# Kernel tuning notes

Hardware: AMD Instinct MI355X
Metric: run time of the kernel (lower is better)

The kernel has to match this reference:

```python
import jax, jax.numpy as jnp
import numpy as np

B, S, D, MP, NA, NC = 32, 1024, 256, 9, 8, 53  # batch, seq, d_model, max_players, n_actions, card vocab


def setup_inputs() -> dict:
    key = jax.random.key(0)
    ks = jax.random.split(key, 24)
    inp = {
        "cards": jax.random.randint(ks[0], (B, S, 7), 0, NC),          # 5 table + 2 hand ids (52 = pad)
        "hero_pos": jax.random.randint(ks[1], (B, S), 0, MP),
        "acting_pos": jax.random.randint(ks[2], (B, S), 0, MP),
        "num_players": jax.random.randint(ks[3], (B, S), 0, MP + 1),
        "scalars": jax.random.normal(ks[4], (B, S, 2), jnp.float32),   # [pot, stack]
        "blinds": jax.random.normal(ks[5], (B, S, 2), jnp.float32),    # [big, small]
        "bets": jax.random.normal(ks[6], (B, S, MP), jnp.float32),
        "action": jax.random.normal(ks[7], (B, S, NA), jnp.float32),
        "mask": jnp.ones((B, S), jnp.float32),
    }
    w = 0.02
    inp.update({
        "card_table": jax.random.normal(ks[8], (NC, D), jnp.float32) * w,
        "hero_table": jax.random.normal(ks[9], (MP, D), jnp.float32) * w,
        "acting_table": jax.random.normal(ks[10], (MP, D), jnp.float32) * w,
        "nump_table": jax.random.normal(ks[11], (MP + 1, D), jnp.float32) * w,
        "scalar_W": jax.random.normal(ks[12], (D, 2), jnp.float32) * w,
        "scalar_b": jax.random.normal(ks[13], (D,), jnp.float32) * w,
        "blind_W": jax.random.normal(ks[14], (D, 2), jnp.float32) * w,
        "blind_b": jax.random.normal(ks[15], (D,), jnp.float32) * w,
        "bet_W": jax.random.normal(ks[16], (D, MP), jnp.float32) * w,
        "bet_b": jax.random.normal(ks[17], (D,), jnp.float32) * w,
        "action_W": jax.random.normal(ks[18], (D, NA), jnp.float32) * w,
        "action_b": jax.random.normal(ks[19], (D,), jnp.float32) * w,
        "combine_W": jax.random.normal(ks[20], (D, 8 * D), jnp.float32) * w,
        "combine_b": jax.random.normal(ks[21], (D,), jnp.float32) * w,
    })
    return inp


def reference(cards, hero_pos, acting_pos, num_players, scalars, blinds, bets, action, mask,
              card_table, hero_table, acting_table, nump_table,
              scalar_W, scalar_b, blind_W, blind_b, bet_W, bet_b,
              action_W, action_b, combine_W, combine_b):
    # Batched gathers (replacing per-event nn.Embedding calls)
    card_emb = card_table[cards].mean(axis=2)          # [B,S,D]
    hero_emb = hero_table[hero_pos]                    # [B,S,D]
    acting_emb = acting_table[acting_pos]              # [B,S,D]
    nump_emb = nump_table[num_players]                 # [B,S,D]
    # Small linear projections (nn.Linear: x @ W.T + b)
    scalar_emb = jnp.einsum('bsk,dk->bsd', scalars, scalar_W) + scalar_b
    blind_emb = jnp.einsum('bsk,dk->bsd', blinds, blind_W) + blind_b
    bet_emb = jnp.einsum('bsk,dk->bsd', bets, bet_W) + bet_b
    action_emb = jnp.einsum('bsk,dk->bsd', action, action_W) + action_b
    # Concat order matches torch: card, hero, acting, scalar, bet, action, num_players, blind
    combined = jnp.concatenate(
        [card_emb, hero_emb, acting_emb, scalar_emb, bet_emb, action_emb, nump_emb, blind_emb],
        axis=-1)                                       # [B,S,8D]
    out = jnp.einsum('bsk,dk->bsd', combined, combine_W) + combine_b  # [B,S,D]
    return out * mask[..., None]                       # zero padded positions
```

## Files before the change

kernel.cpp:

```cpp
#include <hip/hip_runtime.h>

#define D 256
#define W8 2048

#define BPART_OFF 0
#define TBT_OFF   1024
#define KS 136

typedef float nf4  __attribute__((ext_vector_type(4)));
typedef float f32x4 __attribute__((ext_vector_type(4)));
typedef short short8 __attribute__((ext_vector_type(8)));
typedef short short8a2 __attribute__((ext_vector_type(8), aligned(2)));

__device__ __forceinline__ ushort bf16rne(float v) {
    const unsigned x = __float_as_uint(v);
    return (ushort)((x + 0x7fffu + ((x >> 16) & 1u)) >> 16);
}


__global__ __launch_bounds__(256) void fuse5_kernel(
    const float* __restrict__ combine_W,
    const float* __restrict__ card_t, const float* __restrict__ hero_t,
    const float* __restrict__ act_t,  const float* __restrict__ nump_t,
    const float* __restrict__ scalar_W, const float* __restrict__ scalar_b,
    const float* __restrict__ blind_W,  const float* __restrict__ blind_b,
    const float* __restrict__ bet_W,    const float* __restrict__ bet_b,
    const float* __restrict__ action_W, const float* __restrict__ action_b,
    float* __restrict__ ws)
{
    __shared__ float vsh[D];
    __shared__ float Wl[D * 33];

    const int job = blockIdx.x;
    const int tid = threadIdx.x;

    int wblk;
    float scale = 1.0f;
    int kind, orow;

    if (job < 81) {
        kind = 0; orow = job;
        const float* src;
        if (job < 53)      { src = card_t + job * D;        wblk = 0; scale = 1.0f / 7.0f; }
        else if (job < 62) { src = hero_t + (job - 53) * D; wblk = 1; }
        else if (job < 71) { src = act_t  + (job - 62) * D; wblk = 2; }
        else               { src = nump_t + (job - 71) * D; wblk = 6; }
        vsh[tid] = src[tid];
    } else if (job < 102) {
        kind = 1; orow = job - 81;
        const float* secW; int nk, k;
        if (orow < 2)       { secW = scalar_W; nk = 2; k = orow;      wblk = 3; }
        else if (orow < 11) { secW = bet_W;    nk = 9; k = orow - 2;  wblk = 4; }
        else if (orow < 19) { secW = action_W; nk = 8; k = orow - 11; wblk = 5; }
        else                { secW = blind_W;  nk = 2; k = orow - 19; wblk = 7; }
        vsh[tid] = secW[tid * nk + k];
    } else {
        kind = 2; orow = job - 102;
        const float* secB;
        switch (orow) {
            case 0:  secB = scalar_b; wblk = 3; break;
            case 1:  secB = bet_b;    wblk = 4; break;
            case 2:  secB = action_b; wblk = 5; break;
            default: secB = blind_b;  wblk = 7; break;
        }
        vsh[tid] = secB[tid];
    }

    const float* Wbase = combine_W + wblk * D;
    float acc = 0.f;

    for (int t = 0; t < 8; ++t) {
        const int k0 = t * 32;
        __syncthreads();
#pragma unroll
        for (int i = 0; i < 8; ++i) {
            const int fidx = tid + i * 256;
            const int dd = fidx >> 3;
            const int kq = (fidx & 7) * 4;
            const float4 w = *(const float4*)(Wbase + (size_t)dd * W8 + k0 + kq);
            float* p = Wl + dd * 33 + kq;
            p[0] = w.x; p[1] = w.y; p[2] = w.z; p[3] = w.w;
        }
        __syncthreads();
        const float* wrow = Wl + tid * 33;
#pragma unroll
        for (int kk = 0; kk < 32; kk += 4) {
            const float4 vv = *(const float4*)(vsh + k0 + kk);
            acc += wrow[kk]     * vv.x + wrow[kk + 1] * vv.y
                 + wrow[kk + 2] * vv.z + wrow[kk + 3] * vv.w;
        }
    }

    ushort* tbT = (ushort*)(ws + TBT_OFF);
    float*  bpl = ws + BPART_OFF;
    if (kind == 0)      tbT[(size_t)tid * KS + orow]      = bf16rne(acc * scale);
    else if (kind == 1) tbT[(size_t)tid * KS + 81 + orow] = bf16rne(acc);
    else                bpl[orow * D + tid] = acc;
}


#define GEMM_THREADS 256

struct Feat {
    int   c[7], ho, ao, no;
    float fs0, fs1, fb[9], fa[8], fl0, fl1, m;
};

__device__ __forceinline__ void preload(
    int q, int tok, int ok,
    const int* __restrict__ cards,  const int* __restrict__ hero,
    const int* __restrict__ acting, const int* __restrict__ nump,
    const float* __restrict__ scalars, const float* __restrict__ blinds,
    const float* __restrict__ bets,    const float* __restrict__ action,
    const float* __restrict__ mask, Feat& f)
{
    if (!ok) { f.m = 0.f; return; }
    if (q == 0) {
        const int* cp = cards + (size_t)tok * 7;
#pragma unroll
        for (int j = 0; j < 7; ++j) f.c[j] = cp[j];
        f.ho = hero[tok]; f.ao = acting[tok]; f.no = nump[tok];
        f.m = mask[tok];
    } else if (q == 1) {
        const float2 s = *(const float2*)(scalars + (size_t)tok * 2);
        f.fs0 = s.x; f.fs1 = s.y;
        const float* fb = bets + (size_t)tok * 9;
#pragma unroll
        for (int k = 0; k < 9; ++k) f.fb[k] = fb[k];
    } else if (q == 2) {
        const float* fa = action + (size_t)tok * 8;
#pragma unroll
        for (int k = 0; k < 8; ++k) f.fa[k] = fa[k];
        const float2 l = *(const float2*)(blinds + (size_t)tok * 2);
        f.fl0 = l.x; f.fl1 = l.y;
    }
}

__device__ __forceinline__ void writeF(int q, int t, int ok, const Feat& f,
                                       ushort* __restrict__ Fl, float* __restrict__ msk)
{
    ushort* Fr = Fl + t * KS;
    if (q == 0) {
        if (ok) {
            int cnt[7];
#pragma unroll
            for (int j = 0; j < 7; ++j) {
                int n = 1;
#pragma unroll
                for (int i = 0; i < 7; ++i)
                    if (i != j) n += (f.c[i] == f.c[j]) ? 1 : 0;
                cnt[j] = n;
            }
#pragma unroll
            for (int j = 0; j < 7; ++j)
                Fr[f.c[j]] = bf16rne((float)cnt[j]);
            Fr[53 + f.ho] = 0x3F80;
            Fr[62 + f.ao] = 0x3F80;
            Fr[71 + f.no] = 0x3F80;
        }
        msk[t] = f.m;
    } else if (q == 1 && ok) {
        Fr[81] = bf16rne(f.fs0); Fr[82] = bf16rne(f.fs1);
#pragma unroll
        for (int k = 0; k < 9; ++k) Fr[83 + k] = bf16rne(f.fb[k]);
    } else if (q == 2 && ok) {
#pragma unroll
        for (int k = 0; k < 8; ++k) Fr[92 + k] = bf16rne(f.fa[k]);
        Fr[100] = bf16rne(f.fl0); Fr[101] = bf16rne(f.fl1);
    }
}

__device__ __forceinline__ void mfma_tile(
    const ushort* __restrict__ Tg,
    const ushort* __restrict__ Fl,
    const float* __restrict__ msk, const float* __restrict__ bsh,
    int tok0, int h, int w, int lr, int lg,
    float* __restrict__ out, int ntok)
{
    const int nbase = (w >> 1) * 2;
    const int mbase = (w & 1) * 4;

    f32x4 acc[2][4];
#pragma unroll
    for (int nt = 0; nt < 2; ++nt)
#pragma unroll
        for (int mt = 0; mt < 4; ++mt) acc[nt][mt] = (f32x4){0.f, 0.f, 0.f, 0.f};

#pragma unroll
    for (int kt = 0; kt < 4; ++kt) {
        const short8 b0 = *(const short8*)(Fl + ((nbase + 0) * 16 + lr) * KS + kt * 32 + lg * 8);
        const short8 b1 = *(const short8*)(Fl + ((nbase + 1) * 16 + lr) * KS + kt * 32 + lg * 8);
#pragma unroll
        for (int mt = 0; mt < 4; ++mt) {
            const short8 a = *(const short8a2*)(Tg + (size_t)((mbase + mt) * 16 + lr) * KS + kt * 32 + lg * 8);
            acc[0][mt] = __builtin_amdgcn_mfma_f32_16x16x32_bf16(a, b0, acc[0][mt], 0, 0, 0);
            acc[1][mt] = __builtin_amdgcn_mfma_f32_16x16x32_bf16(a, b1, acc[1][mt], 0, 0, 0);
        }
    }

#pragma unroll
    for (int nt = 0; nt < 2; ++nt) {
        const int trow = (nbase + nt) * 16 + lr;
        const int tok = tok0 + trow;
        if (tok < ntok) {
            const float m = msk[trow];
#pragma unroll
            for (int mt = 0; mt < 4; ++mt) {
                const int c = (mbase + mt) * 16 + lg * 4;
                const float4 bb = *(const float4*)(bsh + c);
                nf4 o;
                o.x = (acc[nt][mt][0] + bb.x) * m;
                o.y = (acc[nt][mt][1] + bb.y) * m;
                o.z = (acc[nt][mt][2] + bb.z) * m;
                o.w = (acc[nt][mt][3] + bb.w) * m;
                __builtin_nontemporal_store(o, (nf4*)(out + (size_t)tok * D + h * 128 + c));
            }
        }
    }
}

__global__ __launch_bounds__(GEMM_THREADS) void gemm_kernel(
    const int* __restrict__ cards,  const int* __restrict__ hero,
    const int* __restrict__ acting, const int* __restrict__ nump,
    const float* __restrict__ scalars, const float* __restrict__ blinds,
    const float* __restrict__ bets,    const float* __restrict__ action,
    const float* __restrict__ mask,    const float* __restrict__ combine_b,
    const float* __restrict__ ws, float* __restrict__ out, int ntok)
{
    __shared__ __align__(16) ushort Fl[64 * KS];
    __shared__ float msk[64];
    __shared__ float bsh[128];

    const int tid  = threadIdx.x;
    const int h    = blockIdx.x & 1;
    const int tile = blockIdx.x >> 1;
    const int tok0 = tile * 64;

    const int q = tid >> 6;
    const int t = tid & 63;

    const ushort* Tg = (const ushort*)(ws + TBT_OFF) + (size_t)h * 128 * KS;

    {
        uint* fz = (uint*)Fl;
        for (int i = tid; i < 64 * KS / 2; i += GEMM_THREADS) fz[i] = 0;
        if (tid < 128) {
            const int c = h * 128 + tid;
            bsh[tid] = combine_b[c]
                + ws[BPART_OFF + 0 * D + c] + ws[BPART_OFF + 1 * D + c]
                + ws[BPART_OFF + 2 * D + c] + ws[BPART_OFF + 3 * D + c];
        }
    }
    Feat f;
    preload(q, tok0 + t, tok0 + t < ntok, cards, hero, acting, nump,
            scalars, blinds, bets, action, mask, f);
    __syncthreads();

    writeF(q, t, tok0 + t < ntok, f, Fl, msk);
    __syncthreads();

    const int w  = tid >> 6;
    const int l  = tid & 63;
    const int lr = l & 15;
    const int lg = l >> 4;
    mfma_tile(Tg, Fl, msk, bsh, tok0, h, w, lr, lg, out, ntok);
}

extern "C" void kernel_launch(void* const* d_in, const int* in_sizes, int n_in,
                              void* d_out, int out_size, void* d_ws, size_t ws_size,
                              hipStream_t stream) {
    const int*   cards    = (const int*)d_in[0];
    const int*   hero     = (const int*)d_in[1];
    const int*   acting   = (const int*)d_in[2];
    const int*   nump     = (const int*)d_in[3];
    const float* scalars  = (const float*)d_in[4];
    const float* blinds   = (const float*)d_in[5];
    const float* bets     = (const float*)d_in[6];
    const float* action   = (const float*)d_in[7];
    const float* mask     = (const float*)d_in[8];
    const float* card_t   = (const float*)d_in[9];
    const float* hero_t   = (const float*)d_in[10];
    const float* act_t    = (const float*)d_in[11];
    const float* nump_t   = (const float*)d_in[12];
    const float* scalar_W = (const float*)d_in[13];
    const float* scalar_b = (const float*)d_in[14];
    const float* blind_W  = (const float*)d_in[15];
    const float* blind_b  = (const float*)d_in[16];
    const float* bet_W    = (const float*)d_in[17];
    const float* bet_b    = (const float*)d_in[18];
    const float* action_W = (const float*)d_in[19];
    const float* action_b = (const float*)d_in[20];
    const float* combine_W= (const float*)d_in[21];
    const float* combine_b= (const float*)d_in[22];

    float* ws  = (float*)d_ws;
    float* out = (float*)d_out;
    const int ntok = in_sizes[1];

    const int ntiles = (ntok + 63) / 64;

    hipLaunchKernelGGL(fuse5_kernel, dim3(106), dim3(256), 0, stream,
                       combine_W, card_t, hero_t, act_t, nump_t,
                       scalar_W, scalar_b, blind_W, blind_b, bet_W, bet_b,
                       action_W, action_b, ws);
    hipLaunchKernelGGL(gemm_kernel, dim3(ntiles * 2), dim3(GEMM_THREADS), 0, stream,
                       cards, hero, acting, nump, scalars, blinds, bets, action, mask,
                       combine_b, ws, out, ntok);
}
```

Before: 25.94 us.

## Compute full output width per block to avoid duplicate feature construction

The GEMM kernel used to split the 256 output columns across two blocks per 64-token tile. Each of those blocks rebuilt the same bf16 feature rows in shared memory. Now one block covers all 256 columns: each wave handles 16 tokens against all 16 column tiles, which halves the grid and removes the duplicate gather and preload work. The weight-load vector type is also changed from 2-byte to 16-byte alignment to allow wider loads. In exchange, each wave holds 64 accumulator registers and issues more MFMAs serially, and the smaller grid gives less parallelism to hide latency.

```diff
diff --git a/kernel.cpp b/kernel.cpp
--- a/kernel.cpp
+++ b/kernel.cpp
@@ -10,7 +10,7 @@
 typedef float nf4  __attribute__((ext_vector_type(4)));
 typedef float f32x4 __attribute__((ext_vector_type(4)));
 typedef short short8 __attribute__((ext_vector_type(8)));
-typedef short short8a2 __attribute__((ext_vector_type(8), aligned(2)));
+typedef short short8a16 __attribute__((ext_vector_type(8), aligned(16)));
 
 __device__ __forceinline__ ushort bf16rne(float v) {
     const unsigned x = __float_as_uint(v);
@@ -170,55 +170,6 @@
     }
 }
 
-__device__ __forceinline__ void mfma_tile(
-    const ushort* __restrict__ Tg,
-    const ushort* __restrict__ Fl,
-    const float* __restrict__ msk, const float* __restrict__ bsh,
-    int tok0, int h, int w, int lr, int lg,
-    float* __restrict__ out, int ntok)
-{
-    const int nbase = (w >> 1) * 2;
-    const int mbase = (w & 1) * 4;
-
-    f32x4 acc[2][4];
-#pragma unroll
-    for (int nt = 0; nt < 2; ++nt)
-#pragma unroll
-        for (int mt = 0; mt < 4; ++mt) acc[nt][mt] = (f32x4){0.f, 0.f, 0.f, 0.f};
-
-#pragma unroll
-    for (int kt = 0; kt < 4; ++kt) {
-        const short8 b0 = *(const short8*)(Fl + ((nbase + 0) * 16 + lr) * KS + kt * 32 + lg * 8);
-        const short8 b1 = *(const short8*)(Fl + ((nbase + 1) * 16 + lr) * KS + kt * 32 + lg * 8);
-#pragma unroll
-        for (int mt = 0; mt < 4; ++mt) {
-            const short8 a = *(const short8a2*)(Tg + (size_t)((mbase + mt) * 16 + lr) * KS + kt * 32 + lg * 8);
-            acc[0][mt] = __builtin_amdgcn_mfma_f32_16x16x32_bf16(a, b0, acc[0][mt], 0, 0, 0);
-            acc[1][mt] = __builtin_amdgcn_mfma_f32_16x16x32_bf16(a, b1, acc[1][mt], 0, 0, 0);
-        }
-    }
-
-#pragma unroll
-    for (int nt = 0; nt < 2; ++nt) {
-        const int trow = (nbase + nt) * 16 + lr;
-        const int tok = tok0 + trow;
-        if (tok < ntok) {
-            const float m = msk[trow];
-#pragma unroll
-            for (int mt = 0; mt < 4; ++mt) {
-                const int c = (mbase + mt) * 16 + lg * 4;
-                const float4 bb = *(const float4*)(bsh + c);
-                nf4 o;
-                o.x = (acc[nt][mt][0] + bb.x) * m;
-                o.y = (acc[nt][mt][1] + bb.y) * m;
-                o.z = (acc[nt][mt][2] + bb.z) * m;
-                o.w = (acc[nt][mt][3] + bb.w) * m;
-                __builtin_nontemporal_store(o, (nf4*)(out + (size_t)tok * D + h * 128 + c));
-            }
-        }
-    }
-}
-
 __global__ __launch_bounds__(GEMM_THREADS) void gemm_kernel(
     const int* __restrict__ cards,  const int* __restrict__ hero,
     const int* __restrict__ acting, const int* __restrict__ nump,
@@ -229,27 +180,22 @@
 {
     __shared__ __align__(16) ushort Fl[64 * KS];
     __shared__ float msk[64];
-    __shared__ float bsh[128];
+    __shared__ float bsh[D];
 
     const int tid  = threadIdx.x;
-    const int h    = blockIdx.x & 1;
-    const int tile = blockIdx.x >> 1;
-    const int tok0 = tile * 64;
+    const int tok0 = blockIdx.x * 64;
 
     const int q = tid >> 6;
     const int t = tid & 63;
 
-    const ushort* Tg = (const ushort*)(ws + TBT_OFF) + (size_t)h * 128 * KS;
+    const ushort* Tg = (const ushort*)(ws + TBT_OFF);
 
     {
         uint* fz = (uint*)Fl;
         for (int i = tid; i < 64 * KS / 2; i += GEMM_THREADS) fz[i] = 0;
-        if (tid < 128) {
-            const int c = h * 128 + tid;
-            bsh[tid] = combine_b[c]
-                + ws[BPART_OFF + 0 * D + c] + ws[BPART_OFF + 1 * D + c]
-                + ws[BPART_OFF + 2 * D + c] + ws[BPART_OFF + 3 * D + c];
-        }
+        bsh[tid] = combine_b[tid]
+            + ws[BPART_OFF + 0 * D + tid] + ws[BPART_OFF + 1 * D + tid]
+            + ws[BPART_OFF + 2 * D + tid] + ws[BPART_OFF + 3 * D + tid];
     }
     Feat f;
     preload(q, tok0 + t, tok0 + t < ntok, cards, hero, acting, nump,
@@ -263,7 +209,36 @@
     const int l  = tid & 63;
     const int lr = l & 15;
     const int lg = l >> 4;
-    mfma_tile(Tg, Fl, msk, bsh, tok0, h, w, lr, lg, out, ntok);
+
+    f32x4 acc[16];
+#pragma unroll
+    for (int mt = 0; mt < 16; ++mt) acc[mt] = (f32x4){0.f, 0.f, 0.f, 0.f};
+
+#pragma unroll
+    for (int kt = 0; kt < 4; ++kt) {
+        const short8 b = *(const short8*)(Fl + (w * 16 + lr) * KS + kt * 32 + lg * 8);
+#pragma unroll
+        for (int mt = 0; mt < 16; ++mt) {
+            const short8 a = *(const short8a16*)(Tg + (size_t)(mt * 16 + lr) * KS + kt * 32 + lg * 8);
+            acc[mt] = __builtin_amdgcn_mfma_f32_16x16x32_bf16(a, b, acc[mt], 0, 0, 0);
+        }
+    }
+
+    const int tok = tok0 + w * 16 + lr;
+    if (tok < ntok) {
+        const float m = msk[w * 16 + lr];
+#pragma unroll
+        for (int mt = 0; mt < 16; ++mt) {
+            const int c = mt * 16 + lg * 4;
+            const float4 bb = *(const float4*)(bsh + c);
+            nf4 o;
+            o.x = (acc[mt][0] + bb.x) * m;
+            o.y = (acc[mt][1] + bb.y) * m;
+            o.z = (acc[mt][2] + bb.z) * m;
+            o.w = (acc[mt][3] + bb.w) * m;
+            __builtin_nontemporal_store(o, (nf4*)(out + (size_t)tok * D + c));
+        }
+    }
 }
 
 extern "C" void kernel_launch(void* const* d_in, const int* in_sizes, int n_in,
@@ -303,7 +278,7 @@
                        combine_W, card_t, hero_t, act_t, nump_t,
                        scalar_W, scalar_b, blind_W, blind_b, bet_W, bet_b,
                        action_W, action_b, ws);
-    hipLaunchKernelGGL(gemm_kernel, dim3(ntiles * 2), dim3(GEMM_THREADS), 0, stream,
+    hipLaunchKernelGGL(gemm_kernel, dim3(ntiles), dim3(GEMM_THREADS), 0, stream,
                        cards, hero, acting, nump, scalars, blinds, bets, action, mask,
                        combine_b, ws, out, ntok);
 }
```

Measured after the change: 38.00 us, median of 2. 1.46x slower.
